# Kernel tuning notes

Hardware: AMD Instinct MI355X
Metric: run time of the kernel (lower is better)

The kernel has to match this reference:

```python
import jax, jax.numpy as jnp
import numpy as np

PH, PW = 7, 7            # output_size
SCALE = 0.25             # spatial_scale
SR = 2                   # sampling_ratio (fixed, jit-static)
ALIGNED = True


def setup_inputs() -> dict:
    key = jax.random.key(0)
    k1, k2, k3, k4, k5 = jax.random.split(key, 5)
    B, C, H, W = 4, 256, 200, 200
    N = 512
    img = H / SCALE  # 800.0 image size
    x = jax.random.normal(k1, (B, C, H, W), dtype=jnp.float32)
    bidx = jax.random.randint(k2, (N,), 0, B).astype(jnp.float32)
    cxy = jax.random.uniform(k3, (N, 2), minval=0.0, maxval=img)
    wh = jax.random.uniform(k4, (N, 2), minval=32.0, maxval=256.0)
    x1y1 = jnp.clip(cxy - wh / 2, 0.0, img - 1.0)
    x2y2 = jnp.clip(cxy + wh / 2, 0.0, img - 1.0)
    rois = jnp.concatenate([bidx[:, None], x1y1[:, 0:1], x1y1[:, 1:2],
                            x2y2[:, 0:1], x2y2[:, 1:2]], axis=1).astype(jnp.float32)
    return {"input": x, "rois": rois}


def _axis_samples(start, bin_size, P, size):
    """Sample coords along one axis. start/bin_size: [N]. Returns per-sample
    low/high integer indices, interp weights, and validity mask, all [N, P*SR]."""
    ib = jnp.arange(P, dtype=jnp.float32)           # bin index
    isr = jnp.arange(SR, dtype=jnp.float32)         # sample within bin
    # coord[n, p, s] = start + p*bin + (s+0.5)*bin/SR
    coord = (start[:, None, None]
             + ib[None, :, None] * bin_size[:, None, None]
             + (isr[None, None, :] + 0.5) * bin_size[:, None, None] / SR)
    coord = coord.reshape(coord.shape[0], P * SR)
    valid = (coord >= -1.0) & (coord <= size)
    c = jnp.maximum(coord, 0.0)
    lo_raw = jnp.floor(c).astype(jnp.int32)
    at_edge = lo_raw >= size - 1
    lo = jnp.where(at_edge, size - 1, lo_raw)
    hi = jnp.where(at_edge, size - 1, lo_raw + 1)
    cv = jnp.where(at_edge, jnp.float32(size - 1), c)
    frac = cv - lo.astype(jnp.float32)              # weight toward hi
    return lo, hi, frac, valid


def reference(input, rois):
    B, C, H, W = input.shape
    N = rois.shape[0]
    b = rois[:, 0].astype(jnp.int32)
    off = 0.5 if ALIGNED else 0.0
    sx = rois[:, 1] * SCALE - off
    sy = rois[:, 2] * SCALE - off
    ex = rois[:, 3] * SCALE - off
    ey = rois[:, 4] * SCALE - off
    rw, rh = ex - sx, ey - sy
    if not ALIGNED:
        rw = jnp.maximum(rw, 1.0)
        rh = jnp.maximum(rh, 1.0)
    bin_w, bin_h = rw / PW, rh / PH

    yl, yh, fy, vy = _axis_samples(sy, bin_h, PH, H)   # [N, Sy]
    xl, xh, fx, vx = _axis_samples(sx, bin_w, PW, W)   # [N, Sx]

    featT = jnp.transpose(input, (0, 2, 3, 1))         # [B,H,W,C]

    def gather(yi, xi):  # -> [N, Sy, Sx, C]
        return featT[b[:, None, None], yi[:, :, None], xi[:, None, :]]

    hy, ly = (1.0 - fy), fy
    hx, lx = (1.0 - fx), fx
    w_ll = (hy[:, :, None] * hx[:, None, :])[..., None]
    w_lh = (hy[:, :, None] * lx[:, None, :])[..., None]
    w_hl = (ly[:, :, None] * hx[:, None, :])[..., None]
    w_hh = (ly[:, :, None] * lx[:, None, :])[..., None]

    val = (w_ll * gather(yl, xl) + w_lh * gather(yl, xh)
           + w_hl * gather(yh, xl) + w_hh * gather(yh, xh))
    mask = (vy[:, :, None] & vx[:, None, :])[..., None]
    val = jnp.where(mask, val, 0.0)                    # [N, Sy, Sx, C]

    # average pool the SRxSR samples per output bin
    val = val.reshape(N, PH, SR, PW, SR, C).mean(axis=(2, 4))  # [N,PH,PW,C]
    return jnp.transpose(val, (0, 3, 1, 2))            # [N,C,PH,PW]
```

## Files before the change

### kernel.cpp

```cpp
#include <hip/hip_runtime.h>


#define R_PH 7
#define R_PW 7
#define R_SR 2
#define R_SCALE 0.25f
#define R_C 256
#define R_H 200
#define R_W 200
#define R_HW (R_H * R_W)
#define STRIP 50
#define NSTRIP 4
#define STAGE_ROWS 56

__device__ __forceinline__ void axis_sample(float start, float bin, int p, int s, int size,
                                            int& lo, int& hi, float& wlo, float& whi) {
    float coord = (start + (float)p * bin) + ((float)s + 0.5f) * bin * (1.0f / R_SR);
    bool valid = (coord >= -1.0f) && (coord <= (float)size);
    float c = fmaxf(coord, 0.0f);
    int lo_raw = (int)floorf(c);
    bool at_edge = lo_raw >= size - 1;
    lo = at_edge ? size - 1 : lo_raw;
    hi = at_edge ? size - 1 : lo_raw + 1;
    float cv = at_edge ? (float)(size - 1) : c;
    float frac = cv - (float)lo;
    whi = valid ? frac : 0.0f;
    wlo = valid ? (1.0f - frac) : 0.0f;
}

__global__ void __launch_bounds__(512)
build_lists(const float* __restrict__ rois, int N, int* __restrict__ ws) {
    __shared__ int lcnt[NSTRIP * 4];
    int t = threadIdx.x;
    if (t < 16) lcnt[t] = 0;
    __syncthreads();
    int* lists = ws + 16;
    for (int n = t; n < N; n += 512) {
        const float* r = rois + (size_t)n * 5;
        int b = (int)r[0];
        float sy = r[2] * R_SCALE - 0.5f;
        float ey = r[4] * R_SCALE - 0.5f;
        float binh = (ey - sy) * (1.0f / R_PH);
        for (int ph = 0; ph < R_PH; ++ph) {
            int lo, hi; float wl, wh;
            axis_sample(sy, binh, ph, 0, R_H, lo, hi, wl, wh);
            int bs = b * NSTRIP + lo / STRIP;
            int pos = atomicAdd(&lcnt[bs], 1);
            lists[bs * (N * R_PH) + pos] = (n << 3) | ph;
        }
    }
    __syncthreads();
    if (t < 16) ws[t] = lcnt[t];
}

__global__ void __launch_bounds__(512)
roi_strip(const float* __restrict__ input,
          const float* __restrict__ rois,
          const int* __restrict__ ws, int N,
          float* __restrict__ out) {
    __shared__ float pl[STAGE_ROWS * R_W];
    int c = blockIdx.x;
    int b = blockIdx.y;
    int s = blockIdx.z;

    int m = ws[b * NSTRIP + s];
    if (m == 0) return;

    int r0 = s * STRIP;
    int nrows = min(STAGE_ROWS, R_H - r0);

    const float4* src = (const float4*)(input + (size_t)(b * R_C + c) * R_HW + r0 * R_W);
    float4* dstv = (float4*)pl;
    int nf4 = nrows * (R_W / 4);
    for (int i = threadIdx.x; i < nf4; i += 512) dstv[i] = src[i];

    const int* list = ws + 16 + (b * NSTRIP + s) * (N * R_PH);
    __syncthreads();

    int total = m * R_PW;
    for (int i = threadIdx.x; i < total; i += 512) {
        int e  = i / R_PW;
        int pw = i - e * R_PW;
        int code = list[e];
        int n  = code >> 3;
        int ph = code & 7;
        const float* r = rois + (size_t)n * 5;
        float sx = r[1] * R_SCALE - 0.5f;
        float sy = r[2] * R_SCALE - 0.5f;
        float ex = r[3] * R_SCALE - 0.5f;
        float ey = r[4] * R_SCALE - 0.5f;
        float binw = (ex - sx) * (1.0f / R_PW);
        float binh = (ey - sy) * (1.0f / R_PH);

        int   ylo[R_SR], yhi[R_SR], xlo[R_SR], xhi[R_SR];
        float wyl[R_SR], wyh[R_SR], wxl[R_SR], wxh[R_SR];
#pragma unroll
        for (int q = 0; q < R_SR; ++q) {
            axis_sample(sy, binh, ph, q, R_H, ylo[q], yhi[q], wyl[q], wyh[q]);
            axis_sample(sx, binw, pw, q, R_W, xlo[q], xhi[q], wxl[q], wxh[q]);
        }

        float acc = 0.0f;
#pragma unroll
        for (int ys = 0; ys < R_SR; ++ys) {
            const float* rlo = pl + (ylo[ys] - r0) * R_W;
            const float* rhi = pl + (yhi[ys] - r0) * R_W;
#pragma unroll
            for (int xs = 0; xs < R_SR; ++xs) {
                acc += wyl[ys] * (wxl[xs] * rlo[xlo[xs]] + wxh[xs] * rlo[xhi[xs]])
                     + wyh[ys] * (wxl[xs] * rhi[xlo[xs]] + wxh[xs] * rhi[xhi[xs]]);
            }
        }
        out[(size_t)(n * R_C + c) * 49 + ph * R_PW + pw] = acc * 0.25f;
    }
}

__global__ void __launch_bounds__(256)
roi_align_fwd(const float* __restrict__ input,
              const float* __restrict__ rois,
              float* __restrict__ out, int total) {
    int idx = blockIdx.x * blockDim.x + threadIdx.x;
    if (idx >= total) return;
    int pw = idx % R_PW;
    int ph = (idx / R_PW) % R_PH;
    int c  = (idx / (R_PW * R_PH)) % R_C;
    int n  = idx / (R_PW * R_PH * R_C);
    const float* r = rois + (size_t)n * 5;
    int   b  = (int)r[0];
    float sx = r[1] * R_SCALE - 0.5f;
    float sy = r[2] * R_SCALE - 0.5f;
    float ex = r[3] * R_SCALE - 0.5f;
    float ey = r[4] * R_SCALE - 0.5f;
    float bin_w = (ex - sx) * (1.0f / R_PW);
    float bin_h = (ey - sy) * (1.0f / R_PH);
    const float* plane = input + (size_t)(b * R_C + c) * R_HW;
    int   ylo[R_SR], yhi[R_SR], xlo[R_SR], xhi[R_SR];
    float wylo[R_SR], wyhi[R_SR], wxlo[R_SR], wxhi[R_SR];
#pragma unroll
    for (int s = 0; s < R_SR; ++s) {
        axis_sample(sy, bin_h, ph, s, R_H, ylo[s], yhi[s], wylo[s], wyhi[s]);
        axis_sample(sx, bin_w, pw, s, R_W, xlo[s], xhi[s], wxlo[s], wxhi[s]);
    }
    float acc = 0.0f;
#pragma unroll
    for (int ys = 0; ys < R_SR; ++ys) {
        const float* row_lo = plane + ylo[ys] * R_W;
        const float* row_hi = plane + yhi[ys] * R_W;
#pragma unroll
        for (int xs = 0; xs < R_SR; ++xs) {
            acc += wylo[ys] * (wxlo[xs] * row_lo[xlo[xs]] + wxhi[xs] * row_lo[xhi[xs]])
                 + wyhi[ys] * (wxlo[xs] * row_hi[xlo[xs]] + wxhi[xs] * row_hi[xhi[xs]]);
        }
    }
    out[idx] = acc * (1.0f / (R_SR * R_SR));
}

extern "C" void kernel_launch(void* const* d_in, const int* in_sizes, int n_in,
                              void* d_out, int out_size, void* d_ws, size_t ws_size,
                              hipStream_t stream) {
    const float* input = (const float*)d_in[0];
    const float* rois  = (const float*)d_in[1];
    float* out = (float*)d_out;
    int N = in_sizes[1] / 5;

    size_t ws_needed = (size_t)(16 + 16 * N * R_PH) * sizeof(int);
    if (ws_size >= ws_needed) {
        int* ws = (int*)d_ws;
        build_lists<<<1, 512, 0, stream>>>(rois, N, ws);
        dim3 grid(R_C, 4, NSTRIP);
        roi_strip<<<grid, 512, 0, stream>>>(input, rois, ws, N, out);
    } else {
        int total = out_size;
        roi_align_fwd<<<(total + 255) / 256, 256, 0, stream>>>(input, rois, out, total);
    }
}
```

Baseline: 262.2 us.

## Precompute per-ROI sample tables in setup kernel and shrink strip height

The list-building kernel now precomputes, for each ROI, the x-axis sample indices and weights, plus per-(roi,ph) records holding strip-relative y row offsets, pre-scaled y weights and the output base offset. The strip kernel then only loads these records instead of re-reading the ROI and recomputing the sampling per channel. Strips change from 4x50 rows to 5x40 rows, which cuts the shared-memory staging per block and adds more blocks. The cost is a larger workspace and more global/L2 record reads per item, plus a larger single-block setup kernel.

```diff
diff --git a/kernel.cpp b/kernel.cpp
--- a/kernel.cpp
+++ b/kernel.cpp
@@ -9,9 +9,9 @@
 #define R_H 200
 #define R_W 200
 #define R_HW (R_H * R_W)
-#define STRIP 50
-#define NSTRIP 4
-#define STAGE_ROWS 56
+#define STRIP 40
+#define NSTRIP 5
+#define STAGE_ROWS 46
 
 __device__ __forceinline__ void axis_sample(float start, float bin, int p, int s, int size,
                                             int& lo, int& hi, float& wlo, float& whi) {
@@ -28,42 +28,63 @@
     wlo = valid ? (1.0f - frac) : 0.0f;
 }
 
+
 __global__ void __launch_bounds__(512)
-build_lists(const float* __restrict__ rois, int N, int* __restrict__ ws) {
-    __shared__ int lcnt[NSTRIP * 4];
+build_tables(const float* __restrict__ rois, int N, int* __restrict__ ws) {
+    __shared__ int lcnt[32];
     int t = threadIdx.x;
-    if (t < 16) lcnt[t] = 0;
+    if (t < 32) lcnt[t] = 0;
     __syncthreads();
-    int* lists = ws + 16;
+    float4* xtab = (float4*)(ws + 32);
+    int4*   recs = (int4*)(ws + 32 + N * 56);
     for (int n = t; n < N; n += 512) {
         const float* r = rois + (size_t)n * 5;
         int b = (int)r[0];
+        float sx = r[1] * R_SCALE - 0.5f;
         float sy = r[2] * R_SCALE - 0.5f;
+        float ex = r[3] * R_SCALE - 0.5f;
         float ey = r[4] * R_SCALE - 0.5f;
+        float binw = (ex - sx) * (1.0f / R_PW);
         float binh = (ey - sy) * (1.0f / R_PH);
+        for (int pw = 0; pw < R_PW; ++pw) {
+            for (int q = 0; q < R_SR; ++q) {
+                int lo, hi; float wl, wh;
+                axis_sample(sx, binw, pw, q, R_W, lo, hi, wl, wh);
+                xtab[n * 14 + pw * 2 + q] =
+                    make_float4(__int_as_float(lo), __int_as_float(hi), wl, wh);
+            }
+        }
         for (int ph = 0; ph < R_PH; ++ph) {
-            int lo, hi; float wl, wh;
-            axis_sample(sy, binh, ph, 0, R_H, lo, hi, wl, wh);
-            int bs = b * NSTRIP + lo / STRIP;
+            int lo0, hi0, lo1, hi1; float wl0, wh0, wl1, wh1;
+            axis_sample(sy, binh, ph, 0, R_H, lo0, hi0, wl0, wh0);
+            axis_sample(sy, binh, ph, 1, R_H, lo1, hi1, wl1, wh1);
+            int s  = lo0 / STRIP;
+            int bs = b * NSTRIP + s;
+            int r0 = s * STRIP;
             int pos = atomicAdd(&lcnt[bs], 1);
-            lists[bs * (N * R_PH) + pos] = (n << 3) | ph;
+            int4* rec = recs + ((size_t)bs * N * R_PH + pos) * 3;
+            rec[0] = make_int4(n * 14, n * (R_C * 49) + ph * R_PW,
+                               (lo0 - r0) * R_W, (hi0 - r0) * R_W);
+            rec[1] = make_int4((lo1 - r0) * R_W, (hi1 - r0) * R_W,
+                               __float_as_int(wl0 * 0.25f), __float_as_int(wh0 * 0.25f));
+            rec[2] = make_int4(__float_as_int(wl1 * 0.25f), __float_as_int(wh1 * 0.25f), 0, 0);
         }
     }
     __syncthreads();
-    if (t < 16) ws[t] = lcnt[t];
+    if (t < 32) ws[t] = lcnt[t];
 }
 
 __global__ void __launch_bounds__(512)
 roi_strip(const float* __restrict__ input,
-          const float* __restrict__ rois,
           const int* __restrict__ ws, int N,
           float* __restrict__ out) {
     __shared__ float pl[STAGE_ROWS * R_W];
     int c = blockIdx.x;
     int b = blockIdx.y;
     int s = blockIdx.z;
+    int bs = b * NSTRIP + s;
 
-    int m = ws[b * NSTRIP + s];
+    int m = ws[bs];
     if (m == 0) return;
 
     int r0 = s * STRIP;
@@ -74,44 +95,38 @@
     int nf4 = nrows * (R_W / 4);
     for (int i = threadIdx.x; i < nf4; i += 512) dstv[i] = src[i];
 
-    const int* list = ws + 16 + (b * NSTRIP + s) * (N * R_PH);
+    const float4* xtab = (const float4*)(ws + 32);
+    const int4*   recs = (const int4*)(ws + 32 + N * 56) + (size_t)bs * N * R_PH * 3;
     __syncthreads();
 
     int total = m * R_PW;
+    int cbase = c * 49;
     for (int i = threadIdx.x; i < total; i += 512) {
         int e  = i / R_PW;
         int pw = i - e * R_PW;
-        int code = list[e];
-        int n  = code >> 3;
-        int ph = code & 7;
-        const float* r = rois + (size_t)n * 5;
-        float sx = r[1] * R_SCALE - 0.5f;
-        float sy = r[2] * R_SCALE - 0.5f;
-        float ex = r[3] * R_SCALE - 0.5f;
-        float ey = r[4] * R_SCALE - 0.5f;
-        float binw = (ex - sx) * (1.0f / R_PW);
-        float binh = (ey - sy) * (1.0f / R_PH);
+        int4 ra = recs[e * 3 + 0];
+        int4 rb = recs[e * 3 + 1];
+        int4 rc = recs[e * 3 + 2];
+        float4 xg0 = xtab[ra.x + pw * 2];
+        float4 xg1 = xtab[ra.x + pw * 2 + 1];
+        int xl0 = __float_as_int(xg0.x), xh0 = __float_as_int(xg0.y);
+        int xl1 = __float_as_int(xg1.x), xh1 = __float_as_int(xg1.y);
+        float wxl0 = xg0.z, wxh0 = xg0.w;
+        float wxl1 = xg1.z, wxh1 = xg1.w;
+        const float* rl0 = pl + ra.z;
+        const float* rh0 = pl + ra.w;
+        const float* rl1 = pl + rb.x;
+        const float* rh1 = pl + rb.y;
+        float wyl0 = __int_as_float(rb.z), wyh0 = __int_as_float(rb.w);
+        float wyl1 = __int_as_float(rc.x), wyh1 = __int_as_float(rc.y);
 
-        int   ylo[R_SR], yhi[R_SR], xlo[R_SR], xhi[R_SR];
-        float wyl[R_SR], wyh[R_SR], wxl[R_SR], wxh[R_SR];
-#pragma unroll
-        for (int q = 0; q < R_SR; ++q) {
-            axis_sample(sy, binh, ph, q, R_H, ylo[q], yhi[q], wyl[q], wyh[q]);
-            axis_sample(sx, binw, pw, q, R_W, xlo[q], xhi[q], wxl[q], wxh[q]);
-        }
+        float acc =
+              wyl0 * (wxl0 * rl0[xl0] + wxh0 * rl0[xh0] + wxl1 * rl0[xl1] + wxh1 * rl0[xh1])
+            + wyh0 * (wxl0 * rh0[xl0] + wxh0 * rh0[xh0] + wxl1 * rh0[xl1] + wxh1 * rh0[xh1])
+            + wyl1 * (wxl0 * rl1[xl0] + wxh0 * rl1[xh0] + wxl1 * rl1[xl1] + wxh1 * rl1[xh1])
+            + wyh1 * (wxl0 * rh1[xl0] + wxh0 * rh1[xh0] + wxl1 * rh1[xl1] + wxh1 * rh1[xh1]);
 
-        float acc = 0.0f;
-#pragma unroll
-        for (int ys = 0; ys < R_SR; ++ys) {
-            const float* rlo = pl + (ylo[ys] - r0) * R_W;
-            const float* rhi = pl + (yhi[ys] - r0) * R_W;
-#pragma unroll
-            for (int xs = 0; xs < R_SR; ++xs) {
-                acc += wyl[ys] * (wxl[xs] * rlo[xlo[xs]] + wxh[xs] * rlo[xhi[xs]])
-                     + wyh[ys] * (wxl[xs] * rhi[xlo[xs]] + wxh[xs] * rhi[xhi[xs]]);
-            }
-        }
-        out[(size_t)(n * R_C + c) * 49 + ph * R_PW + pw] = acc * 0.25f;
+        out[ra.y + cbase + pw] = acc;
     }
 }
 
@@ -163,12 +178,13 @@
     float* out = (float*)d_out;
     int N = in_sizes[1] / 5;
 
-    size_t ws_needed = (size_t)(16 + 16 * N * R_PH) * sizeof(int);
+    size_t ws_needed = (size_t)(32 + (size_t)N * 56 +
+                                (size_t)NSTRIP * 4 * N * R_PH * 12) * sizeof(int);
     if (ws_size >= ws_needed) {
         int* ws = (int*)d_ws;
-        build_lists<<<1, 512, 0, stream>>>(rois, N, ws);
+        build_tables<<<1, 512, 0, stream>>>(rois, N, ws);
         dim3 grid(R_C, 4, NSTRIP);
-        roi_strip<<<grid, 512, 0, stream>>>(input, rois, ws, N, out);
+        roi_strip<<<grid, 512, 0, stream>>>(input, ws, N, out);
     } else {
         int total = out_size;
         roi_align_fwd<<<(total + 255) / 256, 256, 0, stream>>>(input, rois, out, total);
```

Result: slower. 272.4 us (+3.9%).
